# Performance work log

Hardware: AMD Instinct MI355X
Metric: run time of the kernel (lower is better)

Reference implementation:

```python
import jax, jax.numpy as jnp
import numpy as np
from jax import lax

B = 2; IMG = 512; P = 16; G = IMG // P; NPATCH = G * G
C = 768; L = 12; HEADS = 12; DH = C // HEADS; SCALE = DH ** -0.5
NQ = 100; PREF = 5; NCLS = 150; NB = 4; NUP = 2
EPS = 1e-6


def _ln(x, w, b, eps=EPS):
    m = x.mean(-1, keepdims=True)
    v = ((x - m) ** 2).mean(-1, keepdims=True)
    return (x - m) * lax.rsqrt(v + eps) * w + b


def _gelu(x):
    return jax.nn.gelu(x, approximate=False)


def setup_inputs() -> dict:
    key = jax.random.key(0)
    ks = iter(jax.random.split(key, 64))
    rn = lambda shape, s=0.02: jax.random.normal(next(ks), shape, jnp.float32) * s
    d = {}
    d['x'] = jax.random.uniform(next(ks), (B, 3, IMG, IMG), jnp.float32, 0.0, 255.0)
    d['pixel_mean'] = jnp.array([0.485, 0.456, 0.406], jnp.float32).reshape(1, 3, 1, 1)
    d['pixel_std'] = jnp.array([0.229, 0.224, 0.225], jnp.float32).reshape(1, 3, 1, 1)
    d['patch_w'] = rn((C, 3 * P * P)); d['patch_b'] = rn((C,))
    d['pos_embed'] = rn((1, NPATCH, C)); d['prefix_tokens'] = rn((PREF, C))
    d['qkv_w'] = rn((L, 3 * C, C)); d['qkv_b'] = rn((L, 3 * C))
    d['proj_w'] = rn((L, C, C)); d['proj_b'] = rn((L, C))
    d['ln1_w'] = jnp.ones((L, C)); d['ln1_b'] = jnp.zeros((L, C))
    d['ln2_w'] = jnp.ones((L, C)); d['ln2_b'] = jnp.zeros((L, C))
    d['ls1'] = jnp.full((L, C), 0.1, jnp.float32); d['ls2'] = jnp.full((L, C), 0.1, jnp.float32)
    d['fc1_w'] = rn((L, 4 * C, C)); d['fc1_b'] = rn((L, 4 * C))
    d['fc2_w'] = rn((L, C, 4 * C)); d['fc2_b'] = rn((L, C))
    d['norm_w'] = jnp.ones((C,)); d['norm_b'] = jnp.zeros((C,))
    d['q_emb'] = rn((NQ, C))
    d['class_w'] = rn((NCLS + 1, C)); d['class_b'] = jnp.zeros((NCLS + 1,))
    d['mh1_w'] = rn((C, C)); d['mh1_b'] = rn((C,))
    d['mh2_w'] = rn((C, C)); d['mh2_b'] = rn((C,))
    d['mh3_w'] = rn((C, C)); d['mh3_b'] = rn((C,))
    d['upt_w'] = rn((NUP, C, C, 2, 2)); d['upt_b'] = rn((NUP, C))
    d['updw_w'] = rn((NUP, C, 1, 3, 3))
    d['upln_w'] = jnp.ones((NUP, C)); d['upln_b'] = jnp.zeros((NUP, C))
    return d


def reference(x, pixel_mean, pixel_std, patch_w, patch_b, pos_embed, prefix_tokens,
              qkv_w, qkv_b, proj_w, proj_b, ln1_w, ln1_b, ln2_w, ln2_b, ls1, ls2,
              fc1_w, fc1_b, fc2_w, fc2_b, norm_w, norm_b, q_emb, class_w, class_b,
              mh1_w, mh1_b, mh2_w, mh2_b, mh3_w, mh3_b, upt_w, upt_b, updw_w,
              upln_w, upln_b):
    Bsz = x.shape[0]
    x = x / 255.0
    x = (x - pixel_mean) / pixel_std
    # patch embed: kernel==stride conv as reshape + matmul -> [B, NPATCH, C]
    x = x.reshape(Bsz, 3, G, P, G, P).transpose(0, 2, 4, 1, 3, 5).reshape(Bsz, NPATCH, 3 * P * P)
    x = x @ patch_w.T + patch_b
    x = x + pos_embed
    x = jnp.concatenate([jnp.broadcast_to(prefix_tokens[None], (Bsz, PREF, C)), x], axis=1)

    def predict(xn):
        q = xn[:, :NQ]
        cls = q @ class_w.T + class_b
        f = xn[:, NQ + PREF:].transpose(0, 2, 1).reshape(Bsz, C, G, G)
        h = _gelu(q @ mh1_w.T + mh1_b)
        h = _gelu(h @ mh2_w.T + mh2_b)
        h = h @ mh3_w.T + mh3_b
        for s in range(NUP):
            Hc, Wc = f.shape[2], f.shape[3]
            # ConvTranspose2d k=2 s=2: each pixel expands to a 2x2 output block
            y = jnp.einsum('bchw,codx->bohdwx', f, upt_w[s])
            f = y.reshape(Bsz, C, 2 * Hc, 2 * Wc) + upt_b[s][None, :, None, None]
            f = _gelu(f)
            f = lax.conv_general_dilated(f, updw_w[s], (1, 1), ((1, 1), (1, 1)),
                                         feature_group_count=C,
                                         dimension_numbers=('NCHW', 'OIHW', 'NCHW'))
            f = _ln(f.transpose(0, 2, 3, 1), upln_w[s], upln_b[s]).transpose(0, 3, 1, 2)
        mlog = jnp.einsum('bqc,bchw->bqhw', h, f)
        return mlog, cls

    mask_list, class_list = [], []
    attn_mask = None
    for i in range(L):
        if i == L - NB:
            x = jnp.concatenate([jnp.broadcast_to(q_emb[None], (Bsz, NQ, C)), x], axis=1)
        if i >= L - NB:
            mlog, clog = predict(_ln(x, norm_w, norm_b))
            mask_list.append(mlog); class_list.append(clog)
            interp = jax.image.resize(mlog, (Bsz, NQ, G, G), method='bilinear')
            qmask = interp.reshape(Bsz, NQ, NPATCH) > 0
            N = x.shape[1]
            attn_mask = jnp.ones((Bsz, N, N), bool).at[:, :NQ, NQ + PREF:].set(qmask)
        N = x.shape[1]
        h = _ln(x, ln1_w[i], ln1_b[i])
        qkv = (h @ qkv_w[i].T + qkv_b[i]).reshape(Bsz, N, 3, HEADS, DH).transpose(2, 0, 3, 1, 4)
        q, k, v = qkv[0], qkv[1], qkv[2]
        s = jnp.einsum('bhnd,bhmd->bhnm', q, k) * SCALE
        if attn_mask is not None:
            s = jnp.where(attn_mask[:, None], s, -jnp.inf)
        a = jax.nn.softmax(s, axis=-1)
        o = jnp.einsum('bhnm,bhmd->bhnd', a, v).transpose(0, 2, 1, 3).reshape(Bsz, N, C)
        x = x + ls1[i] * (o @ proj_w[i].T + proj_b[i])
        h2 = _ln(x, ln2_w[i], ln2_b[i])
        x = x + ls2[i] * (_gelu(h2 @ fc1_w[i].T + fc1_b[i]) @ fc2_w[i].T + fc2_b[i])
    mlog, clog = predict(_ln(x, norm_w, norm_b))
    mask_list.append(mlog); class_list.append(clog)
    return jnp.stack(mask_list), jnp.stack(class_list)
```

## Files before the change

kernel.cpp:

```cpp
#include <hip/hip_runtime.h>
#include <cmath>

namespace {
constexpr int BSZ = 2;
constexpr int IMGSZ = 512;
constexpr int NPATCHES = 1024;
constexpr int CH = 768;
constexpr int LAYERS = 12;
constexpr int DHEAD = 64;
constexpr int NQUERY = 100;
constexpr int NPREFIX = 5;
constexpr int NCLASS = 151;
constexpr int NBLK = 4;
constexpr int NTOK1 = NPREFIX + NPATCHES;
constexpr int NTOK2 = NQUERY + NPREFIX + NPATCHES;
constexpr int QT = 8;
}

typedef unsigned short u16;
typedef __bf16 bf16x8 __attribute__((ext_vector_type(8)));
typedef float floatx4 __attribute__((ext_vector_type(4)));

__device__ __forceinline__ float geluf(float v) {
  return 0.5f * v * (1.0f + erff(v * 0.70710678118654752f));
}
__device__ __forceinline__ u16 f2b(float f) {
  unsigned u = __float_as_uint(f);
  u += 0x7fffu + ((u >> 16) & 1u);
  return (u16)(u >> 16);
}
__device__ __forceinline__ float b2f(u16 v) {
  return __uint_as_float(((unsigned)v) << 16);
}
__device__ __forceinline__ float b2f_lo(unsigned u) {
  return __uint_as_float(u << 16);
}
__device__ __forceinline__ float b2f_hi(unsigned u) {
  return __uint_as_float(u & 0xffff0000u);
}
__device__ __forceinline__ void gl_lds16(const u16* g, u16* l) {
  __builtin_amdgcn_global_load_lds((const __attribute__((address_space(1))) void*)g,
                                   (__attribute__((address_space(3))) void*)l, 16, 0, 0);
}
__device__ __forceinline__ float ldv(const float* p) { return *p; }
__device__ __forceinline__ float ldv(const u16* p) { return b2f(*p); }

__global__ void k_cvt(const float* __restrict__ s, u16* __restrict__ d, int n) {
  int i = (blockIdx.x * 256 + threadIdx.x) * 4;
  if (i >= n) return;
  float4 v = *(const float4*)(s + i);
  u16 r[4] = {f2b(v.x), f2b(v.y), f2b(v.z), f2b(v.w)};
  *(uint2*)(d + i) = *(const uint2*)r;
}

__global__ __launch_bounds__(256) void k_cvt_layer(
    const float* __restrict__ qw, const float* __restrict__ pw,
    const float* __restrict__ f1, const float* __restrict__ f2,
    u16* __restrict__ dq, u16* __restrict__ dp,
    u16* __restrict__ df1, u16* __restrict__ df2) {
  constexpr size_t CC = (size_t)CH * CH;
  size_t i = ((size_t)blockIdx.x * 256 + threadIdx.x) * 8;
  if (i >= 12 * CC) return;
  const float* s; u16* d; size_t o;
  if (i < 3 * CC)      { s = qw; d = dq;  o = i; }
  else if (i < 4 * CC) { s = pw; d = dp;  o = i - 3 * CC; }
  else if (i < 8 * CC) { s = f1; d = df1; o = i - 4 * CC; }
  else                 { s = f2; d = df2; o = i - 8 * CC; }
  float4 a = *(const float4*)(s + o);
  float4 b = *(const float4*)(s + o + 4);
  u16 r[8] = {f2b(a.x), f2b(a.y), f2b(a.z), f2b(a.w),
              f2b(b.x), f2b(b.y), f2b(b.z), f2b(b.w)};
  *(uint4*)(d + o) = *(const uint4*)r;
}

__global__ __launch_bounds__(256) void k_bgemm(
    const u16* __restrict__ A, const u16* __restrict__ B,
    const float* __restrict__ bias,
    float* __restrict__ Cf, u16* __restrict__ Cb,
    int M, int N, int K, int lda, int ldb, int ldcf, int ldcb,
    int flags, int lp2w, const float* __restrict__ lsv) {
  __shared__ u16 As[128 * 32];
  __shared__ u16 Bs[128 * 32];
  const int tid = threadIdx.x;
  const int m0 = blockIdx.y << 7, n0 = blockIdx.x << 7;
  const int wv = tid >> 6, ln = tid & 63;
  const int wm = (wv >> 1) << 6, wn = (wv & 1) << 6;
  const int fr = ln & 15, fq = ln >> 4;
  floatx4 acc[4][4];
#pragma unroll
  for (int i = 0; i < 4; i++)
#pragma unroll
    for (int j = 0; j < 4; j++) acc[i][j] = (floatx4){0.f, 0.f, 0.f, 0.f};

  const int c0 = tid, c1 = tid + 256;
  const u16* Ag0 = A + (size_t)min(m0 + (c0 >> 2), M - 1) * lda + ((c0 & 3) << 3);
  const u16* Ag1 = A + (size_t)min(m0 + (c1 >> 2), M - 1) * lda + ((c1 & 3) << 3);
  const u16* Bg0 = B + (size_t)min(n0 + (c0 >> 2), N - 1) * ldb + ((c0 & 3) << 3);
  const u16* Bg1 = B + (size_t)min(n0 + (c1 >> 2), N - 1) * ldb + ((c1 & 3) << 3);
  u16* Al0 = As + c0 * 8;
  u16* Al1 = As + c1 * 8;
  u16* Bl0 = Bs + c0 * 8;
  u16* Bl1 = Bs + c1 * 8;

  for (int k0 = 0; k0 < K; k0 += 32) {
    gl_lds16(Ag0, Al0);
    gl_lds16(Ag1, Al1);
    gl_lds16(Bg0, Bl0);
    gl_lds16(Bg1, Bl1);
    Ag0 += 32; Ag1 += 32; Bg0 += 32; Bg1 += 32;
    __syncthreads();
    bf16x8 af[4], bb[4];
#pragma unroll
    for (int mi = 0; mi < 4; mi++)
      af[mi] = *(const bf16x8*)(As + ((wm + (mi << 4) + fr) << 5) + (fq << 3));
#pragma unroll
    for (int ni = 0; ni < 4; ni++)
      bb[ni] = *(const bf16x8*)(Bs + ((wn + (ni << 4) + fr) << 5) + (fq << 3));
#pragma unroll
    for (int mi = 0; mi < 4; mi++)
#pragma unroll
      for (int ni = 0; ni < 4; ni++)
        acc[mi][ni] = __builtin_amdgcn_mfma_f32_16x16x32_bf16(af[mi], bb[ni], acc[mi][ni], 0, 0, 0);
    __syncthreads();
  }

#pragma unroll
  for (int mi = 0; mi < 4; mi++) {
#pragma unroll
    for (int ni = 0; ni < 4; ni++) {
#pragma unroll
      for (int r = 0; r < 4; r++) {
        int m = m0 + wm + (mi << 4) + (fq << 2) + r;
        int n = n0 + wn + (ni << 4) + fr;
        if (m >= M || n >= N) continue;
        float v = acc[mi][ni][r];
        if (flags & 2) {
          int o = n % 768, dx = n / 768;
          v = geluf(v + bias[o]);
          int W = 1 << lp2w;
          int y = m >> lp2w, x = m & (W - 1);
          size_t dp = ((size_t)y << (lp2w + 2)) + ((size_t)x << 1) +
                      ((size_t)(dx >> 1) << (lp2w + 1)) + (dx & 1);
          Cb[dp * 768 + o] = f2b(v);
        } else {
          if (bias) v += bias[n];
          if (flags & 1) v = geluf(v);
          if (flags & 4) {
            float* p = Cf + (size_t)m * ldcf + n;
            *p += lsv[n] * v;
          } else {
            if (Cf) Cf[(size_t)m * ldcf + n] = v;
            if (Cb) Cb[(size_t)m * ldcb + n] = f2b(v);
          }
        }
      }
    }
  }
}

template <typename T>
__global__ __launch_bounds__(256) void k_ln(const T* __restrict__ X,
                                            const float* __restrict__ w,
                                            const float* __restrict__ b,
                                            u16* __restrict__ out) {
  const int row = blockIdx.x, tid = threadIdx.x;
  const T* xr = X + (size_t)row * CH;
  float v0 = ldv(xr + tid), v1 = ldv(xr + tid + 256), v2 = ldv(xr + tid + 512);
  float s = v0 + v1 + v2;
  float q = v0 * v0 + v1 * v1 + v2 * v2;
#pragma unroll
  for (int off = 32; off; off >>= 1) {
    s += __shfl_xor(s, off);
    q += __shfl_xor(q, off);
  }
  __shared__ float sh[8];
  const int wv = tid >> 6;
  if ((tid & 63) == 0) { sh[wv] = s; sh[4 + wv] = q; }
  __syncthreads();
  s = (sh[0] + sh[1]) + (sh[2] + sh[3]);
  q = (sh[4] + sh[5]) + (sh[6] + sh[7]);
  float m = s * (1.0f / CH);
  float rstd = rsqrtf(fmaxf(q * (1.0f / CH) - m * m, 0.f) + 1e-6f);
  u16* orow = out + (size_t)row * CH;
  orow[tid]       = f2b((v0 - m) * rstd * w[tid]       + b[tid]);
  orow[tid + 256] = f2b((v1 - m) * rstd * w[tid + 256] + b[tid + 256]);
  orow[tid + 512] = f2b((v2 - m) * rstd * w[tid + 512] + b[tid + 512]);
}

__global__ __launch_bounds__(256) void k_dwln(const u16* __restrict__ in,
                                              const float* __restrict__ w9,
                                              const float* __restrict__ lw,
                                              const float* __restrict__ lb,
                                              u16* __restrict__ out, int H, int W) {
  const int pix = blockIdx.x, tid = threadIdx.x;
  const int x = pix % W, y = pix / W;
  float acc[3];
#pragma unroll
  for (int j = 0; j < 3; j++) {
    const int c = tid + (j << 8);
    const float* wp = w9 + c * 9;
    float sacc = 0.f;
#pragma unroll
    for (int ky = 0; ky < 3; ky++) {
      int yy = y + ky - 1;
      if (yy < 0 || yy >= H) continue;
#pragma unroll
      for (int kx = 0; kx < 3; kx++) {
        int xx = x + kx - 1;
        if (xx < 0 || xx >= W) continue;
        sacc = fmaf(wp[ky * 3 + kx], b2f(in[((size_t)yy * W + xx) * CH + c]), sacc);
      }
    }
    acc[j] = sacc;
  }
  float s = acc[0] + acc[1] + acc[2];
  float q = acc[0] * acc[0] + acc[1] * acc[1] + acc[2] * acc[2];
#pragma unroll
  for (int off = 32; off; off >>= 1) {
    s += __shfl_xor(s, off);
    q += __shfl_xor(q, off);
  }
  __shared__ float sh[8];
  const int wv = tid >> 6;
  if ((tid & 63) == 0) { sh[wv] = s; sh[4 + wv] = q; }
  __syncthreads();
  s = (sh[0] + sh[1]) + (sh[2] + sh[3]);
  q = (sh[4] + sh[5]) + (sh[6] + sh[7]);
  float m = s * (1.0f / CH);
  float rstd = rsqrtf(fmaxf(q * (1.0f / CH) - m * m, 0.f) + 1e-6f);
  u16* orow = out + (size_t)pix * CH;
#pragma unroll
  for (int j = 0; j < 3; j++) {
    const int c = tid + (j << 8);
    orow[c] = f2b((acc[j] - m) * rstd * lw[c] + lb[c]);
  }
}

__global__ __launch_bounds__(256, 4) void k_attn(const u16* __restrict__ qkv,
                                                 u16* __restrict__ out,
                                                 const unsigned char* __restrict__ qm,
                                                 int Ntok) {
  const int b = blockIdx.z, h = blockIdx.y, q0 = blockIdx.x * QT;
  const int tid = threadIdx.x;
  __shared__ float qs[QT][DHEAD];
  __shared__ float srow[QT][1152];
  __shared__ float inv[QT];

  for (int idx = tid; idx < QT * DHEAD; idx += 256) {
    int r = idx >> 6, d = idx & 63;
    float v = 0.f;
    if (q0 + r < Ntok) v = b2f(qkv[(size_t)(b * Ntok + q0 + r) * (3 * CH) + h * DHEAD + d]) * 0.125f;
    qs[r][d] = v;
  }
  __syncthreads();

  const int jj = tid & 63, rg = tid >> 6;
  const u16* kbase = qkv + (size_t)b * Ntok * (3 * CH) + CH + h * DHEAD;

  uint4 cur[8], nxt[8];
  {
    const u16* kp = kbase + (size_t)min(jj, Ntok - 1) * (3 * CH);
#pragma unroll
    for (int i = 0; i < 8; i++) cur[i] = *(const uint4*)(kp + i * 8);
  }
  for (int nb = 0; nb < Ntok; nb += 64) {
    const bool more = (nb + 64 < Ntok);
    if (more) {
      const u16* np = kbase + (size_t)min(nb + 64 + jj, Ntok - 1) * (3 * CH);
#pragma unroll
      for (int i = 0; i < 8; i++) nxt[i] = *(const uint4*)(np + i * 8);
    }
    const int n = nb + jj;
    if (n < Ntok) {
      float a0 = 0.f, a1 = 0.f;
#pragma unroll
      for (int i = 0; i < 8; i++) {
        const int d = i << 3;
        float k0 = b2f_lo(cur[i].x), k1 = b2f_hi(cur[i].x);
        float k2 = b2f_lo(cur[i].y), k3 = b2f_hi(cur[i].y);
        float k4 = b2f_lo(cur[i].z), k5 = b2f_hi(cur[i].z);
        float k6 = b2f_lo(cur[i].w), k7 = b2f_hi(cur[i].w);
        float4 qa0 = *(const float4*)&qs[rg][d];
        float4 qb0 = *(const float4*)&qs[rg + 4][d];
        float4 qa1 = *(const float4*)&qs[rg][d + 4];
        float4 qb1 = *(const float4*)&qs[rg + 4][d + 4];
        a0 = fmaf(k0, qa0.x, a0); a0 = fmaf(k1, qa0.y, a0);
        a0 = fmaf(k2, qa0.z, a0); a0 = fmaf(k3, qa0.w, a0);
        a1 = fmaf(k0, qb0.x, a1); a1 = fmaf(k1, qb0.y, a1);
        a1 = fmaf(k2, qb0.z, a1); a1 = fmaf(k3, qb0.w, a1);
        a0 = fmaf(k4, qa1.x, a0); a0 = fmaf(k5, qa1.y, a0);
        a0 = fmaf(k6, qa1.z, a0); a0 = fmaf(k7, qa1.w, a0);
        a1 = fmaf(k4, qb1.x, a1); a1 = fmaf(k5, qb1.y, a1);
        a1 = fmaf(k6, qb1.z, a1); a1 = fmaf(k7, qb1.w, a1);
      }
      if (qm && n >= NQUERY + NPREFIX) {
        int r0 = q0 + rg, r1 = q0 + rg + 4;
        int pk = n - (NQUERY + NPREFIX);
        if (r0 < NQUERY && !qm[(b * NQUERY + r0) * NPATCHES + pk]) a0 = -1e30f;
        if (r1 < NQUERY && !qm[(b * NQUERY + r1) * NPATCHES + pk]) a1 = -1e30f;
      }
      srow[rg][n] = a0;
      srow[rg + 4][n] = a1;
    }
    if (more) {
#pragma unroll
      for (int i = 0; i < 8; i++) cur[i] = nxt[i];
    }
  }
  __syncthreads();

  {
    const int r = tid >> 5, g = tid & 31;
    float mx = -1e30f;
    for (int n = g; n < Ntok; n += 32) mx = fmaxf(mx, srow[r][n]);
#pragma unroll
    for (int off = 16; off; off >>= 1) mx = fmaxf(mx, __shfl_xor(mx, off));
    float sum = 0.f;
    for (int n = g; n < Ntok; n += 32) {
      float e = __expf(srow[r][n] - mx);
      srow[r][n] = e;
      sum += e;
    }
#pragma unroll
    for (int off = 16; off; off >>= 1) sum += __shfl_xor(sum, off);
    if (g == 0) inv[r] = 1.0f / sum;
  }
  __syncthreads();

  const int d = tid & 63, qr = tid >> 6;
  float oacc[QT];
#pragma unroll
  for (int r = 0; r < QT; r++) oacc[r] = 0.f;
  const u16* vp = qkv + (size_t)b * Ntok * (3 * CH) + 2 * CH + h * DHEAD + d +
                  (size_t)qr * (3 * CH);
  int n = qr;
  for (; n + 12 < Ntok; n += 16) {
    float v0 = b2f(vp[0]);
    float v1 = b2f(vp[4 * 3 * CH]);
    float v2 = b2f(vp[8 * 3 * CH]);
    float v3 = b2f(vp[12 * 3 * CH]);
#pragma unroll
    for (int r = 0; r < QT; r++) oacc[r] = fmaf(srow[r][n], v0, oacc[r]);
#pragma unroll
    for (int r = 0; r < QT; r++) oacc[r] = fmaf(srow[r][n + 4], v1, oacc[r]);
#pragma unroll
    for (int r = 0; r < QT; r++) oacc[r] = fmaf(srow[r][n + 8], v2, oacc[r]);
#pragma unroll
    for (int r = 0; r < QT; r++) oacc[r] = fmaf(srow[r][n + 12], v3, oacc[r]);
    vp += 16 * 3 * CH;
  }
  for (; n < Ntok; n += 4) {
    float vv = b2f(vp[0]);
#pragma unroll
    for (int r = 0; r < QT; r++) oacc[r] = fmaf(srow[r][n], vv, oacc[r]);
    vp += 4 * 3 * CH;
  }
  __syncthreads();
  float* tmp = &srow[0][0];
#pragma unroll
  for (int r = 0; r < QT; r++) tmp[r * 256 + tid] = oacc[r];
  __syncthreads();
#pragma unroll
  for (int p = 0; p < 2; p++) {
    int r = (p << 2) + qr;
    if (q0 + r < Ntok) {
      float t = (tmp[r * 256 + d] + tmp[r * 256 + 64 + d]) +
                (tmp[r * 256 + 128 + d] + tmp[r * 256 + 192 + d]);
      out[(size_t)(b * Ntok + q0 + r) * CH + h * DHEAD + d] = f2b(t * inv[r]);
    }
  }
}

__global__ void k_patchify(const float* __restrict__ x, const float* __restrict__ mean,
                           const float* __restrict__ stdv, u16* __restrict__ xp) {
  int idx = blockIdx.x * 256 + threadIdx.x;
  if (idx >= BSZ * NPATCHES * CH) return;
  int f = idx % CH;
  int p = (idx / CH) % NPATCHES;
  int b = idx / (CH * NPATCHES);
  int c = f >> 8;
  int py = (f >> 4) & 15;
  int px = f & 15;
  int gy = p >> 5, gx = p & 31;
  float v = x[((size_t)(b * 3 + c) * IMGSZ + gy * 16 + py) * IMGSZ + gx * 16 + px];
  xp[idx] = f2b((v * (1.0f / 255.0f) - mean[c]) / stdv[c]);
}

__global__ void k_assemble(const float* __restrict__ xpe, const float* __restrict__ prefix,
                           const float* __restrict__ pos, float* __restrict__ X) {
  int idx = blockIdx.x * 256 + threadIdx.x;
  if (idx >= BSZ * NTOK1 * CH) return;
  int c = idx % CH;
  int n = (idx / CH) % NTOK1;
  int b = idx / (CH * NTOK1);
  float v;
  if (n < NPREFIX) v = prefix[n * CH + c];
  else v = xpe[((size_t)b * NPATCHES + n - NPREFIX) * CH + c] + pos[(size_t)(n - NPREFIX) * CH + c];
  X[idx] = v;
}

__global__ void k_concat(const float* __restrict__ Xin, const float* __restrict__ qe,
                         float* __restrict__ Xout) {
  int idx = blockIdx.x * 256 + threadIdx.x;
  if (idx >= BSZ * NTOK2 * CH) return;
  int c = idx % CH;
  int n = (idx / CH) % NTOK2;
  int b = idx / (CH * NTOK2);
  float v;
  if (n < NQUERY) v = qe[n * CH + c];
  else v = Xin[((size_t)b * NTOK1 + n - NQUERY) * CH + c];
  Xout[idx] = v;
}

__global__ void k_gatherq(const u16* __restrict__ LNb, u16* __restrict__ LNq) {
  int idx = blockIdx.x * 256 + threadIdx.x;
  if (idx >= BSZ * NQUERY * CH) return;
  int c = idx % CH;
  int r = (idx / CH) % NQUERY;
  int b = idx / (CH * NQUERY);
  LNq[idx] = LNb[((size_t)(b * NTOK2 + r)) * CH + c];
}

__global__ __launch_bounds__(256) void k_repack(const float* __restrict__ upt,
                                                u16* __restrict__ WPb) {
  __shared__ float t[4][32][33];
  int o0 = blockIdx.x * 32, c0 = blockIdx.y * 32, s = blockIdx.z;
  int tid = threadIdx.x;
  for (int idx = tid; idx < 32 * 128; idx += 256) {
    int cc = idx >> 7;
    int rest = idx & 127;
    int oo = rest >> 2, dx = rest & 3;
    t[dx][oo][cc] = upt[((size_t)(s * CH + c0 + cc) * CH + o0 + oo) * 4 + dx];
  }
  __syncthreads();
  for (int idx = tid; idx < 4 * 32 * 32; idx += 256) {
    int dx = idx >> 10;
    int oo = (idx >> 5) & 31;
    int cc = idx & 31;
    WPb[((size_t)(s * 4 + dx) * CH + o0 + oo) * CH + c0 + cc] = f2b(t[dx][oo][cc]);
  }
}

__global__ void k_qmask(const float* __restrict__ mlog, unsigned char* __restrict__ qm) {
  int idx = blockIdx.x * 256 + threadIdx.x;
  if (idx >= BSZ * NQUERY * NPATCHES) return;
  int gx = idx & 31;
  int gy = (idx >> 5) & 31;
  int bq = idx >> 10;
  const float* m = mlog + (size_t)bq * 16384;
  float cy = 4.0f * gy + 1.5f, cx = 4.0f * gx + 1.5f;
  int y0 = max(0, 4 * gy - 2), y1 = min(127, 4 * gy + 5);
  int x0 = max(0, 4 * gx - 2), x1 = min(127, 4 * gx + 5);
  float num = 0.f;
  for (int jy = y0; jy <= y1; jy++) {
    float wy = 1.0f - fabsf((float)jy - cy) * 0.25f;
    float rowsum = 0.f;
    for (int jx = x0; jx <= x1; jx++) {
      float wx = 1.0f - fabsf((float)jx - cx) * 0.25f;
      rowsum = fmaf(wx, m[jy * 128 + jx], rowsum);
    }
    num = fmaf(wy, rowsum, num);
  }
  qm[idx] = (num > 0.0f) ? 1 : 0;
}

extern "C" void kernel_launch(void* const* d_in, const int* in_sizes, int n_in,
                              void* d_out_v, int out_size, void* d_ws, size_t ws_size,
                              hipStream_t stream) {
  (void)in_sizes; (void)n_in; (void)out_size; (void)ws_size;
  const float* x_in    = (const float*)d_in[0];
  const float* pmean   = (const float*)d_in[1];
  const float* pstd    = (const float*)d_in[2];
  const float* patch_w = (const float*)d_in[3];
  const float* patch_b = (const float*)d_in[4];
  const float* pos     = (const float*)d_in[5];
  const float* prefix  = (const float*)d_in[6];
  const float* qkv_w   = (const float*)d_in[7];
  const float* qkv_b   = (const float*)d_in[8];
  const float* proj_w  = (const float*)d_in[9];
  const float* proj_b  = (const float*)d_in[10];
  const float* ln1w    = (const float*)d_in[11];
  const float* ln1b    = (const float*)d_in[12];
  const float* ln2w    = (const float*)d_in[13];
  const float* ln2b    = (const float*)d_in[14];
  const float* ls1     = (const float*)d_in[15];
  const float* ls2     = (const float*)d_in[16];
  const float* fc1w    = (const float*)d_in[17];
  const float* fc1b    = (const float*)d_in[18];
  const float* fc2w    = (const float*)d_in[19];
  const float* fc2b    = (const float*)d_in[20];
  const float* normw   = (const float*)d_in[21];
  const float* normb   = (const float*)d_in[22];
  const float* qemb    = (const float*)d_in[23];
  const float* clsw    = (const float*)d_in[24];
  const float* clsb    = (const float*)d_in[25];
  const float* mh1w    = (const float*)d_in[26];
  const float* mh1b    = (const float*)d_in[27];
  const float* mh2w    = (const float*)d_in[28];
  const float* mh2b    = (const float*)d_in[29];
  const float* mh3w    = (const float*)d_in[30];
  const float* mh3b    = (const float*)d_in[31];
  const float* uptw    = (const float*)d_in[32];
  const float* uptb    = (const float*)d_in[33];
  const float* updww   = (const float*)d_in[34];
  const float* uplnw   = (const float*)d_in[35];
  const float* uplnb   = (const float*)d_in[36];

  float* out = (float*)d_out_v;
  float* out_mask = out;
  float* out_cls = out + (size_t)5 * BSZ * NQUERY * 16384;

  char* base = (char*)d_ws;
  size_t off = 0;
  auto allocB = [&](size_t bytes) {
    void* p = base + off;
    off += (bytes + 63) & ~(size_t)63;
    return p;
  };
  float* Xa = (float*)allocB((size_t)BSZ * NTOK2 * CH * 4);
  float* Xb = (float*)allocB((size_t)BSZ * NTOK2 * CH * 4);
  float* Hf = (float*)allocB((size_t)BSZ * NTOK2 * CH * 4);
  u16* Wq  = (u16*)allocB((size_t)3 * CH * CH * 2);
  u16* Wp  = (u16*)allocB((size_t)CH * CH * 2);
  u16* Wf1 = (u16*)allocB((size_t)4 * CH * CH * 2);
  u16* Wf2 = (u16*)allocB((size_t)CH * 4 * CH * 2);
  u16* Wpa = (u16*)allocB((size_t)CH * CH * 2);
  u16* Wcl = (u16*)allocB((size_t)NCLASS * CH * 2);
  u16* Wm1 = (u16*)allocB((size_t)CH * CH * 2);
  u16* Wm2 = (u16*)allocB((size_t)CH * CH * 2);
  u16* Wm3 = (u16*)allocB((size_t)CH * CH * 2);
  u16* WPb = (u16*)allocB((size_t)2 * 4 * CH * CH * 2);
  u16* LNb = (u16*)allocB((size_t)BSZ * NTOK2 * CH * 2);
  u16* AOb = (u16*)allocB((size_t)BSZ * NTOK2 * CH * 2);
  u16* XPb = (u16*)allocB((size_t)BSZ * NPATCHES * CH * 2);
  u16* HQa = (u16*)allocB((size_t)BSZ * NQUERY * CH * 2);
  u16* HQb = (u16*)allocB((size_t)BSZ * NQUERY * CH * 2);
  u16* HQc = (u16*)allocB((size_t)BSZ * NQUERY * CH * 2);
  u16* LNq = (u16*)allocB((size_t)BSZ * NQUERY * CH * 2);
  u16* Sb  = (u16*)allocB((size_t)2 * 16384 * CH * 2);
  unsigned char* QM = (unsigned char*)allocB((size_t)BSZ * NQUERY * NPATCHES);

  u16* QKVb = Sb;
  u16* M1b  = Sb;
  u16* s0g  = Sb;
  u16* s0l  = Sb + (size_t)8192 * CH;
  u16* s1g  = Sb + (size_t)16384 * CH;
  u16* s1d  = Sb;
  u16* s1l  = s1d;

  auto bgemm = [&](const u16* A, const u16* B, const float* bias, float* Cf, u16* Cb,
                   int M, int N, int K, int lda, int ldb, int ldcf, int ldcb,
                   int flags, int lp2w, const float* lsv) {
    dim3 g((N + 127) / 128, (M + 127) / 128);
    k_bgemm<<<g, 256, 0, stream>>>(A, B, bias, Cf, Cb, M, N, K, lda, ldb, ldcf, ldcb,
                                   flags, lp2w, lsv);
  };
  auto cvt = [&](const float* s, u16* d, int n) {
    k_cvt<<<(n / 4 + 255) / 256, 256, 0, stream>>>(s, d, n);
  };
  auto ew = [&](long tot) { return dim3((unsigned)((tot + 255) / 256)); };

  cvt(patch_w, Wpa, CH * CH);
  cvt(clsw, Wcl, NCLASS * CH);
  cvt(mh1w, Wm1, CH * CH);
  cvt(mh2w, Wm2, CH * CH);
  cvt(mh3w, Wm3, CH * CH);
  k_repack<<<dim3(24, 24, 2), 256, 0, stream>>>(uptw, WPb);

  k_patchify<<<ew((long)BSZ * NPATCHES * CH), 256, 0, stream>>>(x_in, pmean, pstd, XPb);
  bgemm(XPb, Wpa, patch_b, Hf, nullptr, BSZ * NPATCHES, CH, CH, CH, CH, CH, 0, 0, 0, nullptr);
  k_assemble<<<ew((long)BSZ * NTOK1 * CH), 256, 0, stream>>>(Hf, prefix, pos, Xa);

  float* X = Xa;
  float* Xalt = Xb;

  auto predict = [&](float* Xcur, int pred, bool build_mask) {
    k_ln<float><<<dim3(BSZ * NTOK2), 256, 0, stream>>>(Xcur, normw, normb, LNb);
    k_gatherq<<<ew((long)BSZ * NQUERY * CH), 256, 0, stream>>>(LNb, LNq);
    bgemm(LNq, Wcl, clsb, out_cls + (size_t)pred * BSZ * NQUERY * NCLASS, nullptr,
          BSZ * NQUERY, NCLASS, CH, CH, CH, NCLASS, 0, 0, 0, nullptr);
    bgemm(LNq, Wm1, mh1b, nullptr, HQa, BSZ * NQUERY, CH, CH, CH, CH, 0, CH, 1, 0, nullptr);
    bgemm(HQa, Wm2, mh2b, nullptr, HQb, BSZ * NQUERY, CH, CH, CH, CH, 0, CH, 1, 0, nullptr);
    bgemm(HQb, Wm3, mh3b, nullptr, HQc, BSZ * NQUERY, CH, CH, CH, CH, 0, CH, 0, 0, nullptr);
    for (int b = 0; b < BSZ; b++) {
      bgemm(LNb + (size_t)(b * NTOK2 + NQUERY + NPREFIX) * CH, WPb, uptb, nullptr, s0g,
            1024, 4 * CH, CH, CH, CH, 0, 0, 2, 5, nullptr);
      k_dwln<<<dim3(4096), 256, 0, stream>>>(s0g, updww, uplnw, uplnb, s0l, 64, 64);
      bgemm(s0l, WPb + (size_t)4 * CH * CH, uptb + CH, nullptr, s1g,
            4096, 4 * CH, CH, CH, CH, 0, 0, 2, 6, nullptr);
      k_dwln<<<dim3(16384), 256, 0, stream>>>(s1g, updww + CH * 9, uplnw + CH, uplnb + CH,
                                              s1l, 128, 128);
      bgemm(HQc + (size_t)b * NQUERY * CH, s1l, nullptr,
            out_mask + (size_t)(pred * BSZ + b) * NQUERY * 16384, nullptr,
            NQUERY, 16384, CH, CH, CH, 16384, 0, 0, 0, nullptr);
    }
    if (build_mask) {
      k_qmask<<<ew((long)BSZ * NQUERY * NPATCHES), 256, 0, stream>>>(
          out_mask + (size_t)pred * BSZ * NQUERY * 16384, QM);
    }
  };

  int Ntok = NTOK1;
  for (int i = 0; i < LAYERS; i++) {
    if (i == LAYERS - NBLK) {
      k_concat<<<ew((long)BSZ * NTOK2 * CH), 256, 0, stream>>>(X, qemb, Xalt);
      float* t = X; X = Xalt; Xalt = t;
      Ntok = NTOK2;
    }
    if (i >= LAYERS - NBLK) predict(X, i - (LAYERS - NBLK), true);
    const int rows = BSZ * Ntok;
    k_cvt_layer<<<dim3(3456), 256, 0, stream>>>(
        qkv_w + (size_t)i * 3 * CH * CH, proj_w + (size_t)i * CH * CH,
        fc1w + (size_t)i * 4 * CH * CH, fc2w + (size_t)i * CH * 4 * CH,
        Wq, Wp, Wf1, Wf2);
    k_ln<float><<<dim3(rows), 256, 0, stream>>>(X, ln1w + i * CH, ln1b + i * CH, LNb);
    bgemm(LNb, Wq, qkv_b + (size_t)i * 3 * CH, nullptr, QKVb,
          rows, 3 * CH, CH, CH, CH, 0, 3 * CH, 0, 0, nullptr);
    k_attn<<<dim3((Ntok + QT - 1) / QT, 12, BSZ), 256, 0, stream>>>(
        QKVb, AOb, (i >= LAYERS - NBLK) ? QM : (const unsigned char*)nullptr, Ntok);
    bgemm(AOb, Wp, proj_b + (size_t)i * CH, X, nullptr,
          rows, CH, CH, CH, CH, CH, 0, 4, 0, ls1 + i * CH);
    k_ln<float><<<dim3(rows), 256, 0, stream>>>(X, ln2w + i * CH, ln2b + i * CH, LNb);
    bgemm(LNb, Wf1, fc1b + (size_t)i * 4 * CH, nullptr, M1b,
          rows, 4 * CH, CH, CH, CH, 0, 4 * CH, 1, 0, nullptr);
    bgemm(M1b, Wf2, fc2b + (size_t)i * CH, X, nullptr,
          rows, CH, 4 * CH, 4 * CH, 4 * CH, CH, 0, 4, 0, ls2 + i * CH);
  }
  predict(X, 4, false);
}
```

Measured before the change: 10.17 ms.

## Batch upscale path across images, fuse final LN with query/patch split, deepen attention prefetch

The upsampling GEMMs and depthwise-conv/LN kernels now process both batch images in a single launch, with batch-aware output indexing in the GEMM scatter epilogue and in k_dwln. The final layernorm writes query and patch rows directly into separate buffers, which removes the gather kernel and the full-token LN buffer. The attention score loop gains triple-buffered K prefetch, and the PV loop is unrolled to 8 loads per step. The scratch buffer grows so the per-batch intermediates no longer alias, which costs more memory and register pressure.

```diff
diff --git a/kernel.cpp b/kernel.cpp
--- a/kernel.cpp
+++ b/kernel.cpp
@@ -138,9 +138,12 @@
           int o = n % 768, dx = n / 768;
           v = geluf(v + bias[o]);
           int W = 1 << lp2w;
-          int y = m >> lp2w, x = m & (W - 1);
+          int bidx = m >> (2 * lp2w);
+          int mloc = m & ((1 << (2 * lp2w)) - 1);
+          int y = mloc >> lp2w, x = mloc & (W - 1);
           size_t dp = ((size_t)y << (lp2w + 2)) + ((size_t)x << 1) +
-                      ((size_t)(dx >> 1) << (lp2w + 1)) + (dx & 1);
+                      ((size_t)(dx >> 1) << (lp2w + 1)) + (dx & 1) +
+                      ((size_t)bidx << (2 * lp2w + 2));
           Cb[dp * 768 + o] = f2b(v);
         } else {
           if (bias) v += bias[n];
@@ -187,12 +190,52 @@
   orow[tid + 512] = f2b((v2 - m) * rstd * w[tid + 512] + b[tid + 512]);
 }
 
+__global__ __launch_bounds__(256) void k_lnp(const float* __restrict__ X,
+                                             const float* __restrict__ w,
+                                             const float* __restrict__ b,
+                                             u16* __restrict__ outq,
+                                             u16* __restrict__ outp) {
+  const int row = blockIdx.x, tid = threadIdx.x;
+  const int bb = row / NTOK2, n = row - bb * NTOK2;
+  u16* orow;
+  if (n < NQUERY) orow = outq + (size_t)(bb * NQUERY + n) * CH;
+  else if (n >= NQUERY + NPREFIX)
+    orow = outp + (size_t)(bb * NPATCHES + (n - NQUERY - NPREFIX)) * CH;
+  else return;
+  const float* xr = X + (size_t)row * CH;
+  float v0 = ldv(xr + tid), v1 = ldv(xr + tid + 256), v2 = ldv(xr + tid + 512);
+  float s = v0 + v1 + v2;
+  float q = v0 * v0 + v1 * v1 + v2 * v2;
+#pragma unroll
+  for (int off = 32; off; off >>= 1) {
+    s += __shfl_xor(s, off);
+    q += __shfl_xor(q, off);
+  }
+  __shared__ float sh[8];
+  const int wv = tid >> 6;
+  if ((tid & 63) == 0) { sh[wv] = s; sh[4 + wv] = q; }
+  __syncthreads();
+  s = (sh[0] + sh[1]) + (sh[2] + sh[3]);
+  q = (sh[4] + sh[5]) + (sh[6] + sh[7]);
+  float m = s * (1.0f / CH);
+  float rstd = rsqrtf(fmaxf(q * (1.0f / CH) - m * m, 0.f) + 1e-6f);
+  orow[tid]       = f2b((v0 - m) * rstd * w[tid]       + b[tid]);
+  orow[tid + 256] = f2b((v1 - m) * rstd * w[tid + 256] + b[tid + 256]);
+  orow[tid + 512] = f2b((v2 - m) * rstd * w[tid + 512] + b[tid + 512]);
+}
+
 __global__ __launch_bounds__(256) void k_dwln(const u16* __restrict__ in,
                                               const float* __restrict__ w9,
                                               const float* __restrict__ lw,
                                               const float* __restrict__ lb,
                                               u16* __restrict__ out, int H, int W) {
-  const int pix = blockIdx.x, tid = threadIdx.x;
+  const int HW = H * W;
+  int pix = blockIdx.x;
+  const int bo = pix / HW;
+  pix -= bo * HW;
+  in += (size_t)bo * HW * CH;
+  out += (size_t)bo * HW * CH;
+  const int tid = threadIdx.x;
   const int x = pix % W, y = pix / W;
   float acc[3];
 #pragma unroll
@@ -257,29 +300,22 @@
   const int jj = tid & 63, rg = tid >> 6;
   const u16* kbase = qkv + (size_t)b * Ntok * (3 * CH) + CH + h * DHEAD;
 
-  uint4 cur[8], nxt[8];
-  {
-    const u16* kp = kbase + (size_t)min(jj, Ntok - 1) * (3 * CH);
-#pragma unroll
-    for (int i = 0; i < 8; i++) cur[i] = *(const uint4*)(kp + i * 8);
-  }
-  for (int nb = 0; nb < Ntok; nb += 64) {
-    const bool more = (nb + 64 < Ntok);
-    if (more) {
-      const u16* np = kbase + (size_t)min(nb + 64 + jj, Ntok - 1) * (3 * CH);
-#pragma unroll
-      for (int i = 0; i < 8; i++) nxt[i] = *(const uint4*)(np + i * 8);
-    }
+  auto LOADC = [&](uint4* buf, int nb) {
+    const u16* p = kbase + (size_t)min(nb + jj, Ntok - 1) * (3 * CH);
+#pragma unroll
+    for (int i = 0; i < 8; i++) buf[i] = *(const uint4*)(p + i * 8);
+  };
+  auto COMP = [&](const uint4* buf, int nb) {
     const int n = nb + jj;
     if (n < Ntok) {
       float a0 = 0.f, a1 = 0.f;
 #pragma unroll
       for (int i = 0; i < 8; i++) {
         const int d = i << 3;
-        float k0 = b2f_lo(cur[i].x), k1 = b2f_hi(cur[i].x);
-        float k2 = b2f_lo(cur[i].y), k3 = b2f_hi(cur[i].y);
-        float k4 = b2f_lo(cur[i].z), k5 = b2f_hi(cur[i].z);
-        float k6 = b2f_lo(cur[i].w), k7 = b2f_hi(cur[i].w);
+        float k0 = b2f_lo(buf[i].x), k1 = b2f_hi(buf[i].x);
+        float k2 = b2f_lo(buf[i].y), k3 = b2f_hi(buf[i].y);
+        float k4 = b2f_lo(buf[i].z), k5 = b2f_hi(buf[i].z);
+        float k6 = b2f_lo(buf[i].w), k7 = b2f_hi(buf[i].w);
         float4 qa0 = *(const float4*)&qs[rg][d];
         float4 qb0 = *(const float4*)&qs[rg + 4][d];
         float4 qa1 = *(const float4*)&qs[rg][d + 4];
@@ -302,9 +338,21 @@
       srow[rg][n] = a0;
       srow[rg + 4][n] = a1;
     }
-    if (more) {
-#pragma unroll
-      for (int i = 0; i < 8; i++) cur[i] = nxt[i];
+  };
+
+  uint4 bA[8], bB[8], bC[8];
+  LOADC(bA, 0);
+  LOADC(bB, 64);
+  for (int nb = 0; nb < Ntok; nb += 192) {
+    LOADC(bC, nb + 128);
+    COMP(bA, nb);
+    if (nb + 64 < Ntok) {
+      LOADC(bA, nb + 192);
+      COMP(bB, nb + 64);
+    }
+    if (nb + 128 < Ntok) {
+      LOADC(bB, nb + 256);
+      COMP(bC, nb + 128);
     }
   }
   __syncthreads();
@@ -334,11 +382,15 @@
   const u16* vp = qkv + (size_t)b * Ntok * (3 * CH) + 2 * CH + h * DHEAD + d +
                   (size_t)qr * (3 * CH);
   int n = qr;
-  for (; n + 12 < Ntok; n += 16) {
+  for (; n + 28 < Ntok; n += 32) {
     float v0 = b2f(vp[0]);
     float v1 = b2f(vp[4 * 3 * CH]);
     float v2 = b2f(vp[8 * 3 * CH]);
     float v3 = b2f(vp[12 * 3 * CH]);
+    float v4 = b2f(vp[16 * 3 * CH]);
+    float v5 = b2f(vp[20 * 3 * CH]);
+    float v6 = b2f(vp[24 * 3 * CH]);
+    float v7 = b2f(vp[28 * 3 * CH]);
 #pragma unroll
     for (int r = 0; r < QT; r++) oacc[r] = fmaf(srow[r][n], v0, oacc[r]);
 #pragma unroll
@@ -347,7 +399,15 @@
     for (int r = 0; r < QT; r++) oacc[r] = fmaf(srow[r][n + 8], v2, oacc[r]);
 #pragma unroll
     for (int r = 0; r < QT; r++) oacc[r] = fmaf(srow[r][n + 12], v3, oacc[r]);
-    vp += 16 * 3 * CH;
+#pragma unroll
+    for (int r = 0; r < QT; r++) oacc[r] = fmaf(srow[r][n + 16], v4, oacc[r]);
+#pragma unroll
+    for (int r = 0; r < QT; r++) oacc[r] = fmaf(srow[r][n + 20], v5, oacc[r]);
+#pragma unroll
+    for (int r = 0; r < QT; r++) oacc[r] = fmaf(srow[r][n + 24], v6, oacc[r]);
+#pragma unroll
+    for (int r = 0; r < QT; r++) oacc[r] = fmaf(srow[r][n + 28], v7, oacc[r]);
+    vp += 32 * 3 * CH;
   }
   for (; n < Ntok; n += 4) {
     float vv = b2f(vp[0]);
@@ -410,15 +470,6 @@
   if (n < NQUERY) v = qe[n * CH + c];
   else v = Xin[((size_t)b * NTOK1 + n - NQUERY) * CH + c];
   Xout[idx] = v;
-}
-
-__global__ void k_gatherq(const u16* __restrict__ LNb, u16* __restrict__ LNq) {
-  int idx = blockIdx.x * 256 + threadIdx.x;
-  if (idx >= BSZ * NQUERY * CH) return;
-  int c = idx % CH;
-  int r = (idx / CH) % NQUERY;
-  int b = idx / (CH * NQUERY);
-  LNq[idx] = LNb[((size_t)(b * NTOK2 + r)) * CH + c];
 }
 
 __global__ __launch_bounds__(256) void k_repack(const float* __restrict__ upt,
@@ -537,16 +588,16 @@
   u16* HQb = (u16*)allocB((size_t)BSZ * NQUERY * CH * 2);
   u16* HQc = (u16*)allocB((size_t)BSZ * NQUERY * CH * 2);
   u16* LNq = (u16*)allocB((size_t)BSZ * NQUERY * CH * 2);
-  u16* Sb  = (u16*)allocB((size_t)2 * 16384 * CH * 2);
+  u16* LNp = (u16*)allocB((size_t)BSZ * NPATCHES * CH * 2);
+  u16* Sb  = (u16*)allocB(((size_t)4 * 4096 * CH + (size_t)4 * 16384 * CH) * 2);
   unsigned char* QM = (unsigned char*)allocB((size_t)BSZ * NQUERY * NPATCHES);
 
+  u16* s0g  = Sb;
+  u16* s0l  = Sb + (size_t)2 * 4096 * CH;
+  u16* s1g  = Sb + (size_t)4 * 4096 * CH;
+  u16* s1d  = s1g + (size_t)2 * 16384 * CH;
   u16* QKVb = Sb;
   u16* M1b  = Sb;
-  u16* s0g  = Sb;
-  u16* s0l  = Sb + (size_t)8192 * CH;
-  u16* s1g  = Sb + (size_t)16384 * CH;
-  u16* s1d  = Sb;
-  u16* s1l  = s1d;
 
   auto bgemm = [&](const u16* A, const u16* B, const float* bias, float* Cf, u16* Cb,
                    int M, int N, int K, int lda, int ldb, int ldcf, int ldcb,
@@ -575,22 +626,21 @@
   float* Xalt = Xb;
 
   auto predict = [&](float* Xcur, int pred, bool build_mask) {
-    k_ln<float><<<dim3(BSZ * NTOK2), 256, 0, stream>>>(Xcur, normw, normb, LNb);
-    k_gatherq<<<ew((long)BSZ * NQUERY * CH), 256, 0, stream>>>(LNb, LNq);
+    k_lnp<<<dim3(BSZ * NTOK2), 256, 0, stream>>>(Xcur, normw, normb, LNq, LNp);
     bgemm(LNq, Wcl, clsb, out_cls + (size_t)pred * BSZ * NQUERY * NCLASS, nullptr,
           BSZ * NQUERY, NCLASS, CH, CH, CH, NCLASS, 0, 0, 0, nullptr);
     bgemm(LNq, Wm1, mh1b, nullptr, HQa, BSZ * NQUERY, CH, CH, CH, CH, 0, CH, 1, 0, nullptr);
     bgemm(HQa, Wm2, mh2b, nullptr, HQb, BSZ * NQUERY, CH, CH, CH, CH, 0, CH, 1, 0, nullptr);
     bgemm(HQb, Wm3, mh3b, nullptr, HQc, BSZ * NQUERY, CH, CH, CH, CH, 0, CH, 0, 0, nullptr);
+    bgemm(LNp, WPb, uptb, nullptr, s0g,
+          BSZ * 1024, 4 * CH, CH, CH, CH, 0, 0, 2, 5, nullptr);
+    k_dwln<<<dim3(BSZ * 4096), 256, 0, stream>>>(s0g, updww, uplnw, uplnb, s0l, 64, 64);
+    bgemm(s0l, WPb + (size_t)4 * CH * CH, uptb + CH, nullptr, s1g,
+          BSZ * 4096, 4 * CH, CH, CH, CH, 0, 0, 2, 6, nullptr);
+    k_dwln<<<dim3(BSZ * 16384), 256, 0, stream>>>(s1g, updww + CH * 9, uplnw + CH,
+                                                  uplnb + CH, s1d, 128, 128);
     for (int b = 0; b < BSZ; b++) {
-      bgemm(LNb + (size_t)(b * NTOK2 + NQUERY + NPREFIX) * CH, WPb, uptb, nullptr, s0g,
-            1024, 4 * CH, CH, CH, CH, 0, 0, 2, 5, nullptr);
-      k_dwln<<<dim3(4096), 256, 0, stream>>>(s0g, updww, uplnw, uplnb, s0l, 64, 64);
-      bgemm(s0l, WPb + (size_t)4 * CH * CH, uptb + CH, nullptr, s1g,
-            4096, 4 * CH, CH, CH, CH, 0, 0, 2, 6, nullptr);
-      k_dwln<<<dim3(16384), 256, 0, stream>>>(s1g, updww + CH * 9, uplnw + CH, uplnb + CH,
-                                              s1l, 128, 128);
-      bgemm(HQc + (size_t)b * NQUERY * CH, s1l, nullptr,
+      bgemm(HQc + (size_t)b * NQUERY * CH, s1d + (size_t)b * 16384 * CH, nullptr,
             out_mask + (size_t)(pred * BSZ + b) * NQUERY * 16384, nullptr,
             NQUERY, 16384, CH, CH, CH, 16384, 0, 0, 0, nullptr);
     }
```

Result: slower. 11.78 ms (+15.9%).
